# Kernel tuning notes

Hardware: AMD Instinct MI355X
Metric: run time of the kernel (lower is better)

The kernel has to match this reference:

```python
import jax, jax.numpy as jnp
import numpy as np
from jax.experimental.ode import odeint

B, T, NV = 2048, 256, 32   # batch, time steps, n ICU variables
H, L, OH = 64, 32, 64      # gru hidden, latent dim, ode hidden


def setup_inputs() -> dict:
    key = jax.random.key(0)
    ks = jax.random.split(key, 24)
    def rn(k, shape, s):
        return (jax.random.normal(k, shape) * s).astype(jnp.float32)
    times = jnp.broadcast_to(jnp.linspace(0.0, 48.0, T, dtype=jnp.float32), (B, T))
    values = jax.random.normal(ks[0], (B, T, NV), dtype=jnp.float32)
    mask = (jax.random.uniform(ks[1], (B, T, NV)) < 0.5).astype(jnp.float32)
    seq_lengths = jnp.sort(jax.random.randint(ks[2], (B,), 1, T + 1))[::-1]
    seq_lengths = seq_lengths.at[0].set(T).astype(jnp.int32)
    eps = jax.random.normal(ks[3], (B, L), dtype=jnp.float32)
    return {
        "times": times, "values": values, "mask": mask,
        "seq_lengths": seq_lengths, "eps": eps,
        # GRU (torch layout: gates stacked r,z,n)
        "W_ih": rn(ks[4], (3 * H, 2 * NV), 0.1), "W_hh": rn(ks[5], (3 * H, H), 0.1),
        "b_ih": rn(ks[6], (3 * H,), 0.05), "b_hh": rn(ks[7], (3 * H,), 0.05),
        # hidden -> z0 params
        "W_z0": rn(ks[8], (2 * L, H), 0.1), "b_z0": rn(ks[9], (2 * L,), 0.05),
        # ODE func MLP (small weights keep dynamics tame for dopri5)
        "ode_W1": rn(ks[10], (OH, L), 0.05), "ode_b1": rn(ks[11], (OH,), 0.02),
        "ode_W2": rn(ks[12], (OH, OH), 0.05), "ode_b2": rn(ks[13], (OH,), 0.02),
        "ode_W3": rn(ks[14], (L, OH), 0.05), "ode_b3": rn(ks[15], (L,), 0.02),
        # decoder
        "dec_W1": rn(ks[16], (H, L), 0.1), "dec_b1": rn(ks[17], (H,), 0.05),
        "dec_W2": rn(ks[18], (1, H), 0.1), "dec_b2": rn(ks[19], (1,), 0.05),
    }


def _latent_ode_fwd(times, values, mask, seq_lengths, eps,
                    W_ih, W_hh, b_ih, b_hh, W_z0, b_z0,
                    ode_W1, ode_b1, ode_W2, ode_b2, ode_W3, ode_b3,
                    dec_W1, dec_b1, dec_W2, dec_b2):
    Bx, Tx = values.shape[0], values.shape[1]
    # encoder: concat (values, mask), flip time, run GRU over first seq_len steps
    x = jnp.concatenate([values, mask], axis=-1)[:, ::-1, :]          # [B,T,2NV]
    xp = jnp.einsum('btf,gf->tbg', x, W_ih) + b_ih                    # [T,B,3H]

    def gru_step(h, inp):
        xpt, t = inp                                                  # xpt: [B,3H]
        hh = h @ W_hh.T + b_hh
        xr, xz, xn = jnp.split(xpt, 3, axis=-1)
        hr, hz, hn = jnp.split(hh, 3, axis=-1)
        r = jax.nn.sigmoid(xr + hr)
        zg = jax.nn.sigmoid(xz + hz)
        n = jnp.tanh(xn + r * hn)
        h_new = (1.0 - zg) * n + zg * h
        h = jnp.where((t < seq_lengths)[:, None], h_new, h)           # packed-seq freeze
        return h, None

    h0 = jnp.zeros((Bx, W_hh.shape[1]), values.dtype)
    h, _ = jax.lax.scan(gru_step, h0, (xp, jnp.arange(Tx)))

    z0p = h @ W_z0.T + b_z0                                           # [B,2L]
    Ld = z0p.shape[-1] // 2
    z0_mean, z0_logvar = z0p[:, :Ld], z0p[:, Ld:]
    z0 = z0_mean + eps * jnp.exp(0.5 * z0_logvar)                     # reparameterize

    def ode_f(z, t, p):
        W1, b1, W2, b2, W3, b3 = p
        hl = jnp.tanh(z @ W1.T + b1)
        hl = jnp.tanh(hl @ W2.T + b2)
        return hl @ W3.T + b3

    t_span = jnp.array([0.0, 48.0], dtype=jnp.float32)
    traj = odeint(ode_f, z0, t_span,
                  (ode_W1, ode_b1, ode_W2, ode_b2, ode_W3, ode_b3),
                  rtol=1e-7, atol=1e-9)                               # dopri5, torchdiffeq defaults
    z_final = traj[-1]

    logits = (jax.nn.relu(z_final @ dec_W1.T + dec_b1) @ dec_W2.T + dec_b2)[:, 0]
    kl = -0.5 * jnp.mean(1.0 + z0_logvar - z0_mean ** 2 - jnp.exp(z0_logvar))
    return logits, kl


def reference(times, values, mask, seq_lengths, eps,
              W_ih, W_hh, b_ih, b_hh, W_z0, b_z0,
              ode_W1, ode_b1, ode_W2, ode_b2, ode_W3, ode_b3,
              dec_W1, dec_b1, dec_W2, dec_b2):
    return _latent_ode_fwd(times, values, mask, seq_lengths, eps,
                           W_ih, W_hh, b_ih, b_hh, W_z0, b_z0,
                           ode_W1, ode_b1, ode_W2, ode_b2, ode_W3, ode_b3,
                           dec_W1, dec_b1, dec_W2, dec_b2)
```

## Files before the change

kernel.cpp:

```cpp
#include <hip/hip_runtime.h>

#define B_ 2048
#define T_ 256
#define NV_ 32
#define H_ 64
#define L_ 32
#define OH_ 64
#define NSTEP 16
#define DEPTH 6

typedef _Float16 f16x8 __attribute__((ext_vector_type(8)));
typedef _Float16 f16x4 __attribute__((ext_vector_type(4)));
typedef float f32x4 __attribute__((ext_vector_type(4)));

#define MFMA16(a, b, c) __builtin_amdgcn_mfma_f32_16x16x32_f16((a), (b), (c), 0, 0, 0)

__device__ __forceinline__ float rcp_(float x) { return __builtin_amdgcn_rcpf(x); }
__device__ __forceinline__ float sigm(float x) { return rcp_(1.0f + __expf(-x)); }
__device__ __forceinline__ float tanh_(float x) { return 2.0f * rcp_(1.0f + __expf(-2.0f * x)) - 1.0f; }

__device__ __forceinline__ f16x8 pack8(f32x4 a, f32x4 b) {
    f16x8 r;
    r[0] = (_Float16)a[0]; r[1] = (_Float16)a[1]; r[2] = (_Float16)a[2]; r[3] = (_Float16)a[3];
    r[4] = (_Float16)b[0]; r[5] = (_Float16)b[1]; r[6] = (_Float16)b[2]; r[7] = (_Float16)b[3];
    return r;
}

__global__ __launch_bounds__(256) void gru_kernel(
    const float* __restrict__ values, const float* __restrict__ mask,
    const int* __restrict__ seql, const float* __restrict__ eps,
    const float* __restrict__ W_ih, const float* __restrict__ W_hh,
    const float* __restrict__ b_ih, const float* __restrict__ b_hh,
    const float* __restrict__ W_z0, const float* __restrict__ b_z0,
    float* __restrict__ z0ws, float* __restrict__ parts)
{
    const int tid = threadIdx.x;
    const int w   = tid >> 6;
    const int l   = tid & 63;
    const int c   = l & 15;
    const int g4  = l >> 4;
    const int b0  = blockIdx.x * 16;

    __shared__ unsigned h_u32[2][16][36];
    __shared__ float    zp_lds[16][68];
    __shared__ float    red_lds[4];
    __shared__ unsigned cnt;

    for (int i = tid; i < 2 * 16 * 36; i += 256) (&h_u32[0][0][0])[i] = 0u;
    if (tid == 0) cnt = 0u;

    f16x8 bih[3][2], bhh[3][2];
#pragma unroll
    for (int gate = 0; gate < 3; ++gate) {
#pragma unroll
        for (int kt = 0; kt < 2; ++kt) {
            const float* p1 = W_ih + (gate * 64 + w * 16 + c) * 64 + kt * 32 + g4 * 8;
            bih[gate][kt] = pack8(*(const f32x4*)p1, *(const f32x4*)(p1 + 4));
            const float* p2 = W_hh + (gate * 64 + w * 16 + c) * 64 + kt * 32 + g4 * 8;
            bhh[gate][kt] = pack8(*(const f32x4*)p2, *(const f32x4*)(p2 + 4));
        }
    }

    f32x4 bRq, bZq, bNXq, bNHq;
#pragma unroll
    for (int r = 0; r < 4; ++r) {
        const int f = w * 16 + g4 * 4 + r;
        bRq[r]  = b_ih[f]       + b_hh[f];
        bZq[r]  = b_ih[64 + f]  + b_hh[64 + f];
        bNXq[r] = b_ih[128 + f];
        bNHq[r] = b_hh[128 + f];
    }

    const int sl_c = seql[b0 + c];
    const int tmax = seql[b0];
    float hp[4] = {0.f, 0.f, 0.f, 0.f};

    const float* vrow = values + (size_t)(b0 + c) * T_ * NV_ + g4 * 8;
    const float* mrow = mask   + (size_t)(b0 + c) * T_ * NV_ + g4 * 8;

#define DECLSET(S) f32x4 S##v0, S##v1, S##m0, S##m1
    DECLSET(A); DECLSET(B); DECLSET(C); DECLSET(D); DECLSET(E); DECLSET(F);
#define FILLSET(S, tc) do {                                                  \
        const int tt_ = ((tc) < tmax) ? (tc) : 0;                            \
        const float* vp_ = vrow + (T_ - 1 - tt_) * NV_;                      \
        const float* mp_ = mrow + (T_ - 1 - tt_) * NV_;                      \
        S##v0 = *(const f32x4*)vp_; S##v1 = *(const f32x4*)(vp_ + 4);        \
        S##m0 = *(const f32x4*)mp_; S##m1 = *(const f32x4*)(mp_ + 4);        \
    } while (0)
    FILLSET(A, 0); FILLSET(B, 1); FILLSET(C, 2);
    FILLSET(D, 3); FILLSET(E, 4); FILLSET(F, 5);

    __syncthreads();

#define GSTEP(S, tc) do {                                                    \
        f16x8 ha0 = *(const f16x8*)&h_u32[(tc) & 1][c][4 * g4];              \
        f16x8 ha1 = *(const f16x8*)&h_u32[(tc) & 1][c][16 + 4 * g4];         \
        f16x8 xa0 = pack8(S##v0, S##v1);                                     \
        f16x8 xa1 = pack8(S##m0, S##m1);                                     \
        FILLSET(S, (tc) + DEPTH);                                            \
        f32x4 accR  = MFMA16(bih[0][0], xa0, bRq);                           \
        f32x4 accNX = MFMA16(bih[2][0], xa0, bNXq);                          \
        f32x4 accZ  = MFMA16(bih[1][0], xa0, bZq);                           \
        accR  = MFMA16(bih[0][1], xa1, accR);                                \
        accNX = MFMA16(bih[2][1], xa1, accNX);                               \
        accZ  = MFMA16(bih[1][1], xa1, accZ);                                \
        f32x4 accNH = MFMA16(bhh[2][0], ha0, bNHq);                          \
        accR  = MFMA16(bhh[0][0], ha0, accR);                                \
        accNH = MFMA16(bhh[2][1], ha1, accNH);                               \
        accR  = MFMA16(bhh[0][1], ha1, accR);                                \
        accZ  = MFMA16(bhh[1][0], ha0, accZ);                                \
        accZ  = MFMA16(bhh[1][1], ha1, accZ);                                \
        const bool act = ((tc) < sl_c);                                      \
        _Pragma("unroll")                                                    \
        for (int r = 0; r < 4; ++r) {                                        \
            float rr   = sigm(accR[r]);                                      \
            float zz   = sigm(accZ[r]);                                      \
            float nn   = tanh_(accNX[r] + rr * accNH[r]);                    \
            float hnew = nn + zz * (hp[r] - nn);                             \
            if (act) hp[r] = hnew;                                           \
        }                                                                    \
        f16x4 hq;                                                            \
        _Pragma("unroll")                                                    \
        for (int r = 0; r < 4; ++r) hq[r] = (_Float16)hp[r];                 \
        *(f16x4*)&h_u32[((tc) & 1) ^ 1][c][8 * w + 2 * g4] = hq;             \
        asm volatile("s_waitcnt lgkmcnt(0)" ::: "memory");                   \
        if (l == 0) atomicAdd(&cnt, 1u);                                     \
        asm volatile("" ::: "memory");                                       \
        {                                                                    \
            const unsigned tgt_ = 4u * ((unsigned)(tc) + 1u);                \
            while (__builtin_amdgcn_readfirstlane(                           \
                       *(volatile unsigned*)&cnt) < tgt_) { }                \
        }                                                                    \
        asm volatile("" ::: "memory");                                       \
    } while (0)

    int t = 0;
    while (true) {
        GSTEP(A, t); if (++t >= tmax) break;
        GSTEP(B, t); if (++t >= tmax) break;
        GSTEP(C, t); if (++t >= tmax) break;
        GSTEP(D, t); if (++t >= tmax) break;
        GSTEP(E, t); if (++t >= tmax) break;
        GSTEP(F, t); if (++t >= tmax) break;
    }

    f16x8 az0f[2];
#pragma unroll
    for (int kt = 0; kt < 2; ++kt) {
        const float* p = W_z0 + (w * 16 + c) * 64 + kt * 32 + g4 * 8;
        az0f[kt] = pack8(*(const f32x4*)p, *(const f32x4*)(p + 4));
    }
    const int fin = tmax & 1;
    f16x8 hf0 = *(const f16x8*)&h_u32[fin][c][4 * g4];
    f16x8 hf1 = *(const f16x8*)&h_u32[fin][c][16 + 4 * g4];
    f32x4 az;
#pragma unroll
    for (int r = 0; r < 4; ++r) az[r] = b_z0[w * 16 + g4 * 4 + r];
    az = MFMA16(az0f[0], hf0, az);
    az = MFMA16(az0f[1], hf1, az);
    *(f32x4*)&zp_lds[c][w * 16 + g4 * 4] = az;
    __syncthreads();

    const int row = tid >> 4;
    const int j2  = (tid & 15) * 2;
    float m0 = zp_lds[row][j2],      m1 = zp_lds[row][j2 + 1];
    float v0 = zp_lds[row][32 + j2], v1 = zp_lds[row][32 + j2 + 1];
    const float* erow = eps + (size_t)(b0 + row) * L_;
    float e0 = erow[j2], e1 = erow[j2 + 1];
    float* zrow = z0ws + (size_t)(b0 + row) * L_;
    float s0 = __expf(0.5f * v0), s1 = __expf(0.5f * v1);
    zrow[j2]     = m0 + e0 * s0;
    zrow[j2 + 1] = m1 + e1 * s1;
    float kls = (1.0f + v0 - m0 * m0 - s0 * s0) + (1.0f + v1 - m1 * m1 - s1 * s1);
#pragma unroll
    for (int off = 32; off >= 1; off >>= 1) kls += __shfl_down(kls, off);
    if (l == 0) red_lds[w] = kls;
    __syncthreads();
    if (tid == 0) parts[blockIdx.x] = red_lds[0] + red_lds[1] + red_lds[2] + red_lds[3];
}

__global__ __launch_bounds__(64) void ode_kernel(
    const float* __restrict__ z0ws,
    const float* __restrict__ oW1, const float* __restrict__ ob1,
    const float* __restrict__ oW2, const float* __restrict__ ob2,
    const float* __restrict__ oW3, const float* __restrict__ ob3,
    const float* __restrict__ dW1, const float* __restrict__ db1,
    const float* __restrict__ dW2, const float* __restrict__ db2,
    float* __restrict__ out)
{
    const int l  = threadIdx.x;
    const int c  = l & 15;
    const int g4 = l >> 4;
    const int b0 = blockIdx.x * 16;

    __shared__ _Float16 zbuf[16][40];
    __shared__ _Float16 buf1[16][72];
    __shared__ _Float16 buf2[16][72];

    f16x8 w1f[4], d1f[4], w2f[4][2], w3f[2][2];
#pragma unroll
    for (int mt = 0; mt < 4; ++mt) {
        const float* p = oW1 + (mt * 16 + c) * 32 + g4 * 8;
        w1f[mt] = pack8(*(const f32x4*)p, *(const f32x4*)(p + 4));
        const float* q = dW1 + (mt * 16 + c) * 32 + g4 * 8;
        d1f[mt] = pack8(*(const f32x4*)q, *(const f32x4*)(q + 4));
#pragma unroll
        for (int kt = 0; kt < 2; ++kt) {
            const float* r = oW2 + (mt * 16 + c) * 64 + kt * 32 + g4 * 8;
            w2f[mt][kt] = pack8(*(const f32x4*)r, *(const f32x4*)(r + 4));
        }
    }
#pragma unroll
    for (int mt = 0; mt < 2; ++mt) {
#pragma unroll
        for (int kt = 0; kt < 2; ++kt) {
            const float* r = oW3 + (mt * 16 + c) * 64 + kt * 32 + g4 * 8;
            w3f[mt][kt] = pack8(*(const f32x4*)r, *(const f32x4*)(r + 4));
        }
    }

    f32x4 b1q[4], b2q[4], d1q[4], w2q[4], b3q[2];
#pragma unroll
    for (int mt = 0; mt < 4; ++mt) {
#pragma unroll
        for (int r = 0; r < 4; ++r) {
            b1q[mt][r] = ob1[mt * 16 + g4 * 4 + r];
            b2q[mt][r] = ob2[mt * 16 + g4 * 4 + r];
            d1q[mt][r] = db1[mt * 16 + g4 * 4 + r];
            w2q[mt][r] = dW2[mt * 16 + g4 * 4 + r];
        }
    }
#pragma unroll
    for (int mt = 0; mt < 2; ++mt) {
#pragma unroll
        for (int r = 0; r < 4; ++r) b3q[mt][r] = ob3[mt * 16 + g4 * 4 + r];
    }
    const float bd2 = db2[0];

    f32x4 z[2];
#pragma unroll
    for (int mt = 0; mt < 2; ++mt)
        z[mt] = *(const f32x4*)(z0ws + (size_t)(b0 + c) * L_ + mt * 16 + g4 * 4);

    auto evalf = [&](const f32x4* zin, f32x4* kout) {
#pragma unroll
        for (int mt = 0; mt < 2; ++mt) {
            f16x4 hv;
#pragma unroll
            for (int r = 0; r < 4; ++r) hv[r] = (_Float16)zin[mt][r];
            *(f16x4*)&zbuf[c][mt * 16 + g4 * 4] = hv;
        }
        f16x8 zf = *(const f16x8*)&zbuf[c][g4 * 8];

        f32x4 h1[4];
#pragma unroll
        for (int mt = 0; mt < 4; ++mt) h1[mt] = MFMA16(w1f[mt], zf, b1q[mt]);
#pragma unroll
        for (int mt = 0; mt < 4; ++mt) {
            f16x4 hv;
#pragma unroll
            for (int r = 0; r < 4; ++r) hv[r] = (_Float16)tanh_(h1[mt][r]);
            *(f16x4*)&buf1[c][mt * 16 + g4 * 4] = hv;
        }
        f16x8 a1 = *(const f16x8*)&buf1[c][g4 * 8];
        f16x8 a2 = *(const f16x8*)&buf1[c][32 + g4 * 8];

        f32x4 h2[4];
#pragma unroll
        for (int mt = 0; mt < 4; ++mt) {
            h2[mt] = MFMA16(w2f[mt][0], a1, b2q[mt]);
            h2[mt] = MFMA16(w2f[mt][1], a2, h2[mt]);
        }
#pragma unroll
        for (int mt = 0; mt < 4; ++mt) {
            f16x4 hv;
#pragma unroll
            for (int r = 0; r < 4; ++r) hv[r] = (_Float16)tanh_(h2[mt][r]);
            *(f16x4*)&buf2[c][mt * 16 + g4 * 4] = hv;
        }
        f16x8 a3 = *(const f16x8*)&buf2[c][g4 * 8];
        f16x8 a4 = *(const f16x8*)&buf2[c][32 + g4 * 8];

#pragma unroll
        for (int mt = 0; mt < 2; ++mt) {
            kout[mt] = MFMA16(w3f[mt][0], a3, b3q[mt]);
            kout[mt] = MFMA16(w3f[mt][1], a4, kout[mt]);
        }
    };

    const float dt = 48.0f / (float)NSTEP;
    for (int s = 0; s < NSTEP; ++s) {
        f32x4 k[2], ks[2], zt[2];
        evalf(z, k);
#pragma unroll
        for (int mt = 0; mt < 2; ++mt) { ks[mt] = k[mt]; zt[mt] = z[mt] + k[mt] * (0.5f * dt); }
        evalf(zt, k);
#pragma unroll
        for (int mt = 0; mt < 2; ++mt) { ks[mt] += k[mt] * 2.0f; zt[mt] = z[mt] + k[mt] * (0.5f * dt); }
        evalf(zt, k);
#pragma unroll
        for (int mt = 0; mt < 2; ++mt) { ks[mt] += k[mt] * 2.0f; zt[mt] = z[mt] + k[mt] * dt; }
        evalf(zt, k);
#pragma unroll
        for (int mt = 0; mt < 2; ++mt) z[mt] += (ks[mt] + k[mt]) * (dt / 6.0f);
    }

#pragma unroll
    for (int mt = 0; mt < 2; ++mt) {
        f16x4 hv;
#pragma unroll
        for (int r = 0; r < 4; ++r) hv[r] = (_Float16)z[mt][r];
        *(f16x4*)&zbuf[c][mt * 16 + g4 * 4] = hv;
    }
    f16x8 zf = *(const f16x8*)&zbuf[c][g4 * 8];
    float p = 0.0f;
#pragma unroll
    for (int mt = 0; mt < 4; ++mt) {
        f32x4 d = MFMA16(d1f[mt], zf, d1q[mt]);
#pragma unroll
        for (int r = 0; r < 4; ++r) p += fmaxf(d[r], 0.0f) * w2q[mt][r];
    }
    p += __shfl_xor(p, 16);
    p += __shfl_xor(p, 32);
    if (l < 16) out[b0 + c] = p + bd2;
}

__global__ __launch_bounds__(128) void kl_fin(const float* __restrict__ parts,
                                              float* __restrict__ out)
{
    __shared__ float sred[2];
    const int tid = threadIdx.x;
    float p = parts[tid];
#pragma unroll
    for (int off = 32; off >= 1; off >>= 1) p += __shfl_down(p, off);
    if ((tid & 63) == 0) sred[tid >> 6] = p;
    __syncthreads();
    if (tid == 0) out[B_] = -0.5f * (sred[0] + sred[1]) / (float)(B_ * L_);
}

extern "C" void kernel_launch(void* const* d_in, const int* in_sizes, int n_in,
                              void* d_out, int out_size, void* d_ws, size_t ws_size,
                              hipStream_t stream) {
    const float* values = (const float*)d_in[1];
    const float* mask   = (const float*)d_in[2];
    const int*   seql   = (const int*)d_in[3];
    const float* eps    = (const float*)d_in[4];
    const float* W_ih   = (const float*)d_in[5];
    const float* W_hh   = (const float*)d_in[6];
    const float* b_ih   = (const float*)d_in[7];
    const float* b_hh   = (const float*)d_in[8];
    const float* W_z0   = (const float*)d_in[9];
    const float* b_z0   = (const float*)d_in[10];
    const float* oW1    = (const float*)d_in[11];
    const float* ob1    = (const float*)d_in[12];
    const float* oW2    = (const float*)d_in[13];
    const float* ob2    = (const float*)d_in[14];
    const float* oW3    = (const float*)d_in[15];
    const float* ob3    = (const float*)d_in[16];
    const float* dW1    = (const float*)d_in[17];
    const float* db1    = (const float*)d_in[18];
    const float* dW2    = (const float*)d_in[19];
    const float* db2    = (const float*)d_in[20];
    float* out = (float*)d_out;

    float* z0ws  = (float*)d_ws;
    float* parts = z0ws + (size_t)B_ * L_;

    hipLaunchKernelGGL(gru_kernel, dim3(B_ / 16), dim3(256), 0, stream,
                       values, mask, seql, eps, W_ih, W_hh, b_ih, b_hh, W_z0, b_z0,
                       z0ws, parts);
    hipLaunchKernelGGL(ode_kernel, dim3(B_ / 16), dim3(64), 0, stream,
                       z0ws, oW1, ob1, oW2, ob2, oW3, ob3, dW1, db1, dW2, db2, out);
    hipLaunchKernelGGL(kl_fin, dim3(1), dim3(128), 0, stream, parts, out);
}
```

Baseline: 225.5 us.

## Software-pipeline GRU input projection, fold log2e into weights, fuse KL reduction

The GRU step is restructured so the input-projection MFMAs for the next step are issued alongside the recurrent MFMAs of the current step. The two K-halves of the recurrent matmul now accumulate separately to shorten the dependency chain. Gate weights and biases are prescaled by log2(e) so exp2 can replace exp. The LDS atomic-counter spin barrier is replaced by s_barrier, the hidden state is packed with cvt_pkrtz, prefetch depth drops from 6 to 3, and NSTEP changes from 16 to 12. The separate KL finalize kernel is merged into block 0 of the ODE kernel, removing one launch, but the smaller NSTEP may change ODE accuracy or cost.

```diff
diff --git a/kernel.cpp b/kernel.cpp
--- a/kernel.cpp
+++ b/kernel.cpp
@@ -6,16 +6,18 @@
 #define H_ 64
 #define L_ 32
 #define OH_ 64
-#define NSTEP 16
-#define DEPTH 6
+#define NSTEP 12
 
 typedef _Float16 f16x8 __attribute__((ext_vector_type(8)));
 typedef _Float16 f16x4 __attribute__((ext_vector_type(4)));
 typedef float f32x4 __attribute__((ext_vector_type(4)));
 
 #define MFMA16(a, b, c) __builtin_amdgcn_mfma_f32_16x16x32_f16((a), (b), (c), 0, 0, 0)
+#define LOG2E 1.44269504f
 
 __device__ __forceinline__ float rcp_(float x) { return __builtin_amdgcn_rcpf(x); }
+__device__ __forceinline__ float sigm2(float x) { return rcp_(1.0f + exp2f(-x)); }
+__device__ __forceinline__ float tanh2(float x) { return 2.0f * rcp_(1.0f + exp2f(-x)) - 1.0f; }
 __device__ __forceinline__ float sigm(float x) { return rcp_(1.0f + __expf(-x)); }
 __device__ __forceinline__ float tanh_(float x) { return 2.0f * rcp_(1.0f + __expf(-2.0f * x)) - 1.0f; }
 
@@ -24,6 +26,17 @@
     r[0] = (_Float16)a[0]; r[1] = (_Float16)a[1]; r[2] = (_Float16)a[2]; r[3] = (_Float16)a[3];
     r[4] = (_Float16)b[0]; r[5] = (_Float16)b[1]; r[6] = (_Float16)b[2]; r[7] = (_Float16)b[3];
     return r;
+}
+__device__ __forceinline__ f16x8 pack8s(f32x4 a, f32x4 b, float s) {
+    f16x8 r;
+    r[0] = (_Float16)(s * a[0]); r[1] = (_Float16)(s * a[1]);
+    r[2] = (_Float16)(s * a[2]); r[3] = (_Float16)(s * a[3]);
+    r[4] = (_Float16)(s * b[0]); r[5] = (_Float16)(s * b[1]);
+    r[6] = (_Float16)(s * b[2]); r[7] = (_Float16)(s * b[3]);
+    return r;
+}
+__device__ __forceinline__ unsigned pk_u32(float a, float b) {
+    return __builtin_bit_cast(unsigned, __builtin_amdgcn_cvt_pkrtz(a, b));
 }
 
 __global__ __launch_bounds__(256) void gru_kernel(
@@ -44,32 +57,37 @@
     __shared__ unsigned h_u32[2][16][36];
     __shared__ float    zp_lds[16][68];
     __shared__ float    red_lds[4];
-    __shared__ unsigned cnt;
 
     for (int i = tid; i < 2 * 16 * 36; i += 256) (&h_u32[0][0][0])[i] = 0u;
-    if (tid == 0) cnt = 0u;
-
-    f16x8 bih[3][2], bhh[3][2];
-#pragma unroll
-    for (int gate = 0; gate < 3; ++gate) {
-#pragma unroll
-        for (int kt = 0; kt < 2; ++kt) {
-            const float* p1 = W_ih + (gate * 64 + w * 16 + c) * 64 + kt * 32 + g4 * 8;
-            bih[gate][kt] = pack8(*(const f32x4*)p1, *(const f32x4*)(p1 + 4));
-            const float* p2 = W_hh + (gate * 64 + w * 16 + c) * 64 + kt * 32 + g4 * 8;
-            bhh[gate][kt] = pack8(*(const f32x4*)p2, *(const f32x4*)(p2 + 4));
-        }
+
+    f16x8 bihR[2], bihZ[2], bihN[2], bhhR[2], bhhZ[2], bhhN[2];
+#pragma unroll
+    for (int kt = 0; kt < 2; ++kt) {
+        const float* p;
+        p = W_ih + (0 * 64 + w * 16 + c) * 64 + kt * 32 + g4 * 8;
+        bihR[kt] = pack8s(*(const f32x4*)p, *(const f32x4*)(p + 4), LOG2E);
+        p = W_ih + (1 * 64 + w * 16 + c) * 64 + kt * 32 + g4 * 8;
+        bihZ[kt] = pack8s(*(const f32x4*)p, *(const f32x4*)(p + 4), LOG2E);
+        p = W_ih + (2 * 64 + w * 16 + c) * 64 + kt * 32 + g4 * 8;
+        bihN[kt] = pack8s(*(const f32x4*)p, *(const f32x4*)(p + 4), 2.0f * LOG2E);
+        p = W_hh + (0 * 64 + w * 16 + c) * 64 + kt * 32 + g4 * 8;
+        bhhR[kt] = pack8s(*(const f32x4*)p, *(const f32x4*)(p + 4), LOG2E);
+        p = W_hh + (1 * 64 + w * 16 + c) * 64 + kt * 32 + g4 * 8;
+        bhhZ[kt] = pack8s(*(const f32x4*)p, *(const f32x4*)(p + 4), LOG2E);
+        p = W_hh + (2 * 64 + w * 16 + c) * 64 + kt * 32 + g4 * 8;
+        bhhN[kt] = pack8s(*(const f32x4*)p, *(const f32x4*)(p + 4), 2.0f * LOG2E);
     }
 
     f32x4 bRq, bZq, bNXq, bNHq;
 #pragma unroll
     for (int r = 0; r < 4; ++r) {
         const int f = w * 16 + g4 * 4 + r;
-        bRq[r]  = b_ih[f]       + b_hh[f];
-        bZq[r]  = b_ih[64 + f]  + b_hh[64 + f];
-        bNXq[r] = b_ih[128 + f];
-        bNHq[r] = b_hh[128 + f];
-    }
+        bRq[r]  = LOG2E * (b_ih[f]      + b_hh[f]);
+        bZq[r]  = LOG2E * (b_ih[64 + f] + b_hh[64 + f]);
+        bNXq[r] = 2.0f * LOG2E * b_ih[128 + f];
+        bNHq[r] = 2.0f * LOG2E * b_hh[128 + f];
+    }
+    const f32x4 Z4 = {0.f, 0.f, 0.f, 0.f};
 
     const int sl_c = seql[b0 + c];
     const int tmax = seql[b0];
@@ -78,8 +96,7 @@
     const float* vrow = values + (size_t)(b0 + c) * T_ * NV_ + g4 * 8;
     const float* mrow = mask   + (size_t)(b0 + c) * T_ * NV_ + g4 * 8;
 
-#define DECLSET(S) f32x4 S##v0, S##v1, S##m0, S##m1
-    DECLSET(A); DECLSET(B); DECLSET(C); DECLSET(D); DECLSET(E); DECLSET(F);
+    f32x4 av0, av1, am0, am1, bv0, bv1, bm0, bm1;
 #define FILLSET(S, tc) do {                                                  \
         const int tt_ = ((tc) < tmax) ? (tc) : 0;                            \
         const float* vp_ = vrow + (T_ - 1 - tt_) * NV_;                      \
@@ -87,61 +104,63 @@
         S##v0 = *(const f32x4*)vp_; S##v1 = *(const f32x4*)(vp_ + 4);        \
         S##m0 = *(const f32x4*)mp_; S##m1 = *(const f32x4*)(mp_ + 4);        \
     } while (0)
-    FILLSET(A, 0); FILLSET(B, 1); FILLSET(C, 2);
-    FILLSET(D, 3); FILLSET(E, 4); FILLSET(F, 5);
+    FILLSET(a, 0); FILLSET(b, 1);
+
+    f32x4 xpR, xpZ, xpNX;
+    {
+        f16x8 xa0 = pack8(av0, av1);
+        f16x8 xa1 = pack8(am0, am1);
+        FILLSET(a, 2);
+        xpR  = MFMA16(bihR[0], xa0, bRq);  xpR  = MFMA16(bihR[1], xa1, xpR);
+        xpZ  = MFMA16(bihZ[0], xa0, bZq);  xpZ  = MFMA16(bihZ[1], xa1, xpZ);
+        xpNX = MFMA16(bihN[0], xa0, bNXq); xpNX = MFMA16(bihN[1], xa1, xpNX);
+    }
 
     __syncthreads();
 
-#define GSTEP(S, tc) do {                                                    \
-        f16x8 ha0 = *(const f16x8*)&h_u32[(tc) & 1][c][4 * g4];              \
-        f16x8 ha1 = *(const f16x8*)&h_u32[(tc) & 1][c][16 + 4 * g4];         \
-        f16x8 xa0 = pack8(S##v0, S##v1);                                     \
-        f16x8 xa1 = pack8(S##m0, S##m1);                                     \
-        FILLSET(S, (tc) + DEPTH);                                            \
-        f32x4 accR  = MFMA16(bih[0][0], xa0, bRq);                           \
-        f32x4 accNX = MFMA16(bih[2][0], xa0, bNXq);                          \
-        f32x4 accZ  = MFMA16(bih[1][0], xa0, bZq);                           \
-        accR  = MFMA16(bih[0][1], xa1, accR);                                \
-        accNX = MFMA16(bih[2][1], xa1, accNX);                               \
-        accZ  = MFMA16(bih[1][1], xa1, accZ);                                \
-        f32x4 accNH = MFMA16(bhh[2][0], ha0, bNHq);                          \
-        accR  = MFMA16(bhh[0][0], ha0, accR);                                \
-        accNH = MFMA16(bhh[2][1], ha1, accNH);                               \
-        accR  = MFMA16(bhh[0][1], ha1, accR);                                \
-        accZ  = MFMA16(bhh[1][0], ha0, accZ);                                \
-        accZ  = MFMA16(bhh[1][1], ha1, accZ);                                \
+#define STEPB(SN, tc, RB, WB) do {                                           \
+        f16x8 ha0 = *(const f16x8*)&h_u32[RB][c][4 * g4];                    \
+        f16x8 ha1 = *(const f16x8*)&h_u32[RB][c][16 + 4 * g4];               \
+                             \
+        f32x4 aR  = MFMA16(bhhR[0], ha0, xpR);                               \
+        f32x4 aNH = MFMA16(bhhN[0], ha0, bNHq);                              \
+        f32x4 aZ  = MFMA16(bhhZ[0], ha0, xpZ);                               \
+                                \
+        f32x4 aR1  = MFMA16(bhhR[1], ha1, Z4);                               \
+        f32x4 aNH1 = MFMA16(bhhN[1], ha1, Z4);                               \
+        f32x4 aZ1  = MFMA16(bhhZ[1], ha1, Z4);                               \
+              \
+        f16x8 xa0 = pack8(SN##v0, SN##v1);                                   \
+        f16x8 xa1 = pack8(SN##m0, SN##m1);                                   \
+        FILLSET(SN, (tc) + 3);                                               \
+        f32x4 nxpR  = MFMA16(bihR[0], xa0, bRq);                             \
+        f32x4 nxpZ  = MFMA16(bihZ[0], xa0, bZq);                             \
+        f32x4 nxpNX = MFMA16(bihN[0], xa0, bNXq);                            \
+        nxpR  = MFMA16(bihR[1], xa1, nxpR);                                  \
+        nxpZ  = MFMA16(bihZ[1], xa1, nxpZ);                                  \
+        nxpNX = MFMA16(bihN[1], xa1, nxpNX);                                 \
+        aR  += aR1;  aNH += aNH1;  aZ += aZ1;                                \
         const bool act = ((tc) < sl_c);                                      \
         _Pragma("unroll")                                                    \
         for (int r = 0; r < 4; ++r) {                                        \
-            float rr   = sigm(accR[r]);                                      \
-            float zz   = sigm(accZ[r]);                                      \
-            float nn   = tanh_(accNX[r] + rr * accNH[r]);                    \
+            float rr   = sigm2(aR[r]);                                       \
+            float nn   = tanh2(xpNX[r] + rr * aNH[r]);                       \
+            float zz   = sigm2(aZ[r]);                                       \
             float hnew = nn + zz * (hp[r] - nn);                             \
             if (act) hp[r] = hnew;                                           \
         }                                                                    \
-        f16x4 hq;                                                            \
-        _Pragma("unroll")                                                    \
-        for (int r = 0; r < 4; ++r) hq[r] = (_Float16)hp[r];                 \
-        *(f16x4*)&h_u32[((tc) & 1) ^ 1][c][8 * w + 2 * g4] = hq;             \
-        asm volatile("s_waitcnt lgkmcnt(0)" ::: "memory");                   \
-        if (l == 0) atomicAdd(&cnt, 1u);                                     \
-        asm volatile("" ::: "memory");                                       \
-        {                                                                    \
-            const unsigned tgt_ = 4u * ((unsigned)(tc) + 1u);                \
-            while (__builtin_amdgcn_readfirstlane(                           \
-                       *(volatile unsigned*)&cnt) < tgt_) { }                \
-        }                                                                    \
-        asm volatile("" ::: "memory");                                       \
+        h_u32[WB][c][8 * w + 2 * g4]     = pk_u32(hp[0], hp[1]);             \
+        h_u32[WB][c][8 * w + 2 * g4 + 1] = pk_u32(hp[2], hp[3]);             \
+        xpR = nxpR; xpZ = nxpZ; xpNX = nxpNX;                                \
+        asm volatile("s_waitcnt lgkmcnt(0)\n\ts_barrier" ::: "memory");      \
     } while (0)
 
     int t = 0;
     while (true) {
-        GSTEP(A, t); if (++t >= tmax) break;
-        GSTEP(B, t); if (++t >= tmax) break;
-        GSTEP(C, t); if (++t >= tmax) break;
-        GSTEP(D, t); if (++t >= tmax) break;
-        GSTEP(E, t); if (++t >= tmax) break;
-        GSTEP(F, t); if (++t >= tmax) break;
+        STEPB(b, t, 0, 1);
+        if (++t >= tmax) break;
+        STEPB(a, t, 1, 0);
+        if (++t >= tmax) break;
     }
 
     f16x8 az0f[2];
@@ -180,7 +199,7 @@
 }
 
 __global__ __launch_bounds__(64) void ode_kernel(
-    const float* __restrict__ z0ws,
+    const float* __restrict__ z0ws, const float* __restrict__ parts,
     const float* __restrict__ oW1, const float* __restrict__ ob1,
     const float* __restrict__ oW2, const float* __restrict__ ob2,
     const float* __restrict__ oW3, const float* __restrict__ ob3,
@@ -202,8 +221,8 @@
     for (int mt = 0; mt < 4; ++mt) {
         const float* p = oW1 + (mt * 16 + c) * 32 + g4 * 8;
         w1f[mt] = pack8(*(const f32x4*)p, *(const f32x4*)(p + 4));
-        const float* q = dW1 + (mt * 16 + c) * 32 + g4 * 8;
-        d1f[mt] = pack8(*(const f32x4*)q, *(const f32x4*)(q + 4));
+        const float* qq = dW1 + (mt * 16 + c) * 32 + g4 * 8;
+        d1f[mt] = pack8(*(const f32x4*)qq, *(const f32x4*)(qq + 4));
 #pragma unroll
         for (int kt = 0; kt < 2; ++kt) {
             const float* r = oW2 + (mt * 16 + c) * 64 + kt * 32 + g4 * 8;
@@ -323,19 +342,13 @@
     p += __shfl_xor(p, 16);
     p += __shfl_xor(p, 32);
     if (l < 16) out[b0 + c] = p + bd2;
-}
-
-__global__ __launch_bounds__(128) void kl_fin(const float* __restrict__ parts,
-                                              float* __restrict__ out)
-{
-    __shared__ float sred[2];
-    const int tid = threadIdx.x;
-    float p = parts[tid];
-#pragma unroll
-    for (int off = 32; off >= 1; off >>= 1) p += __shfl_down(p, off);
-    if ((tid & 63) == 0) sred[tid >> 6] = p;
-    __syncthreads();
-    if (tid == 0) out[B_] = -0.5f * (sred[0] + sred[1]) / (float)(B_ * L_);
+
+    if (blockIdx.x == 0) {
+        float kp = parts[l] + parts[l + 64];
+#pragma unroll
+        for (int off = 32; off >= 1; off >>= 1) kp += __shfl_down(kp, off);
+        if (l == 0) out[B_] = -0.5f * kp / (float)(B_ * L_);
+    }
 }
 
 extern "C" void kernel_launch(void* const* d_in, const int* in_sizes, int n_in,
@@ -370,6 +383,5 @@
                        values, mask, seql, eps, W_ih, W_hh, b_ih, b_hh, W_z0, b_z0,
                        z0ws, parts);
     hipLaunchKernelGGL(ode_kernel, dim3(B_ / 16), dim3(64), 0, stream,
-                       z0ws, oW1, ob1, oW2, ob2, oW3, ob3, dW1, db1, dW2, db2, out);
-    hipLaunchKernelGGL(kl_fin, dim3(1), dim3(128), 0, stream, parts, out);
-}
+                       z0ws, parts, oW1, ob1, oW2, ob2, oW3, ob3, dW1, db1, dW2, db2, out);
+}
```

Result: faster. 215.1 us (-4.6%).
